# Performance work log

Hardware: AMD Instinct MI355X
Metric: run time of the kernel (lower is better)

Reference implementation:

```python
import jax, jax.numpy as jnp
import numpy as np

K_NEIGH = 12
RADIUS = 0.5


def _mlp(x, w1, b1, w2, b2):
    return jax.nn.relu(x @ w1 + b1) @ w2 + b2


def _angle(a, b):
    # atan2(||a x b||, a.b), as in PyG point-pair features
    c = jnp.cross(a, b)
    return jnp.arctan2(jnp.linalg.norm(c, axis=-1), jnp.sum(a * b, axis=-1))


def _quat_to_mat(q):
    w, x, y, z = q[:, 0], q[:, 1], q[:, 2], q[:, 3]
    m = jnp.stack([
        1 - 2 * (y * y + z * z), 2 * (x * y - z * w), 2 * (x * z + y * w),
        2 * (x * y + z * w), 1 - 2 * (x * x + z * z), 2 * (y * z - x * w),
        2 * (x * z - y * w), 2 * (y * z + x * w), 1 - 2 * (x * x + y * y),
    ], axis=-1)
    return m.reshape(-1, 3, 3)


def _lin_params(key, fan_in, fan_out):
    kw, kb = jax.random.split(key)
    s = 1.0 / np.sqrt(fan_in)
    w = jax.random.uniform(kw, (fan_in, fan_out), minval=-s, maxval=s, dtype=jnp.float32)
    b = jax.random.uniform(kb, (fan_out,), minval=-s, maxval=s, dtype=jnp.float32)
    return w, b


def setup_inputs() -> dict:
    key = jax.random.key(0)
    keys = jax.random.split(key, 8)
    points = jax.random.uniform(keys[0], (1, 128, 64, 3), dtype=jnp.float32)
    dims = [(7, 32, 16), (19, 32, 8), (24, 32, 16), (16, 32, 8), (24, 32, 16), (16, 32, 12), (27, 64, 1)]
    names = ['l1', 'g1', 'l2', 'g2', 'l3', 'g3', 'l4']
    inp = {'points': points}
    for i, (nm, (di, dh, do)) in enumerate(zip(names, dims)):
        k1, k2 = jax.random.split(keys[i + 1])
        w1, b1 = _lin_params(k1, di, dh)
        w2, b2 = _lin_params(k2, dh, do)
        inp[nm + '_w1'], inp[nm + '_b1'], inp[nm + '_w2'], inp[nm + '_b2'] = w1, b1, w2, b2
    return inp


def reference(points, l1_w1, l1_b1, l1_w2, l1_b2, g1_w1, g1_b1, g1_w2, g1_b2,
              l2_w1, l2_b1, l2_w2, l2_b2, g2_w1, g2_b1, g2_w2, g2_b2,
              l3_w1, l3_b1, l3_w2, l3_b2, g3_w1, g3_b1, g3_w2, g3_b2,
              l4_w1, l4_b1, l4_w2, l4_b2):
    B, H, W, _ = points.shape
    pos = points.reshape(-1, 3)          # [N,3]
    N = pos.shape[0]
    K = K_NEIGH
    pos_sg = jax.lax.stop_gradient(pos)  # torch detaches pos before edge features

    # --- dense radius graph: K nearest neighbors, self-padded beyond radius ---
    sq = jnp.sum(pos_sg * pos_sg, -1)
    d2 = sq[:, None] + sq[None, :] - 2.0 * (pos_sg @ pos_sg.T)  # [N,N]
    idx = jnp.arange(N)
    d2 = d2.at[idx, idx].set(jnp.inf)
    neg_d2_k, knn = jax.lax.top_k(-d2, K)
    d2_k = -neg_d2_k
    dense = jnp.where(d2_k <= RADIUS * RADIUS, knn, idx[:, None])  # [N,K]
    rows = jnp.repeat(idx, K)            # [E]
    cols = dense.reshape(-1)             # [E]

    # --- covariance of neighborhood, analytic 3x3 eig -> PCA normals ---
    nbr = pos[dense]                     # [N,K,3] (non-detached, as in torch)
    cent = jnp.mean(nbr, axis=1, keepdims=True)
    diff = nbr - cent
    cov = jnp.einsum('nki,nkj->nij', diff, diff) / K
    noise = (jax.random.uniform(jax.random.key(42), (100, 3), dtype=jnp.float32) - 0.5) * 1e-8
    cov = cov + jnp.diag(noise)          # torch.diag of (100,3) -> length-3 vector broadcast
    eig_val, eig_vec = jnp.linalg.eigh(cov)  # ascending, matches sort+gather in torch
    normals = eig_vec[:, :, 0]           # eigenvector of smallest eigenvalue
    pca_normals = normals.reshape(B, H, W, 3).transpose(0, 3, 1, 2)

    # --- edge feature stack: gather-MLP-mean-broadcast chain ---
    cart = pos_sg[cols] - pos_sg[rows]   # [E,3]
    dist = jnp.linalg.norm(cart, axis=-1)
    n_r, n_c = normals[rows], normals[cols]
    ppf = jnp.stack([dist, _angle(n_r, cart), _angle(n_c, cart), _angle(n_r, n_c)], -1)
    x = _mlp(jnp.concatenate([cart, ppf], -1), l1_w1, l1_b1, l1_w2, l1_b2)  # [E,16]

    gx = jnp.concatenate([x.reshape(N, K, -1).mean(1), normals], -1)        # [N,19]
    x_g = _mlp(gx, g1_w1, g1_b1, g1_w2, g1_b2)                              # [N,8]
    x = _mlp(jnp.concatenate([x, x_g[rows]], 1), l2_w1, l2_b1, l2_w2, l2_b2)

    x_g = _mlp(x.reshape(N, K, -1).mean(1), g2_w1, g2_b1, g2_w2, g2_b2)
    x = _mlp(jnp.concatenate([x, x_g[rows]], 1), l3_w1, l3_b1, l3_w2, l3_b2)

    x_g = _mlp(x.reshape(N, K, -1).mean(1), g3_w1, g3_b1, g3_w2, g3_b2)     # [N,12]
    quat = x_g[:, :4]
    quat = quat / (jnp.linalg.norm(quat, axis=-1) + 1e-8)[:, None]
    mat = _quat_to_mat(quat)             # [N,3,3]
    feat_g = x_g[:, 4:]
    rot_cart = jnp.einsum('eij,ej->ei', mat[rows], cart)
    x = _mlp(jnp.concatenate([x, feat_g[rows], rot_cart], 1), l4_w1, l4_b1, l4_w2, l4_b2)

    point_fea = jax.nn.softmax(x.reshape(N, K), axis=1)
    point_fea = point_fea.reshape(B, H, W, K).transpose(0, 3, 1, 2)
    return pca_normals, point_fea
```

## Files before the change

### kernel.cpp

```cpp
#include <hip/hip_runtime.h>
#include <math.h>

#define KNB 12
#define GRD 8
#define NCELL (GRD * GRD * GRD)


__device__ __forceinline__ unsigned umin32(unsigned a, unsigned b) {
    unsigned r; asm("v_min_u32 %0, %1, %2" : "=v"(r) : "v"(a), "v"(b)); return r;
}
__device__ __forceinline__ unsigned umax32(unsigned a, unsigned b) {
    unsigned r; asm("v_max_u32 %0, %1, %2" : "=v"(r) : "v"(a), "v"(b)); return r;
}

__device__ __forceinline__ float fm(float a, float b) { return __fmul_rn(a, b); }
__device__ __forceinline__ float fa(float a, float b) { return __fadd_rn(a, b); }
__device__ __forceinline__ float fs(float a, float b) { return __fsub_rn(a, b); }
__device__ __forceinline__ float fsignf(float a, float b) { return (b >= 0.0f) ? fabsf(a) : -fabsf(a); }

__device__ float slapy2_(float x, float y) {
    float xa = fabsf(x), ya = fabsf(y);
    float w = fmaxf(xa, ya), z = fminf(xa, ya);
    if (z == 0.0f) return w;
    float q = z / w;
    return fm(w, __fsqrt_rn(fa(1.0f, fm(q, q))));
}

__device__ void slartg_(float f, float g, float& c, float& s, float& r) {
    if (g == 0.0f) { c = 1.0f; s = 0.0f; r = f; }
    else if (f == 0.0f) { c = 0.0f; s = (g >= 0.0f) ? 1.0f : -1.0f; r = fabsf(g); }
    else {
        float d = __fsqrt_rn(fa(fm(f, f), fm(g, g)));
        c = fabsf(f) / d;
        r = (f >= 0.0f) ? d : -d;
        s = g / r;
    }
}

__device__ void slaev2_(float a, float b, float cc,
                        float& rt1, float& rt2, float& cs1, float& sn1) {
    float sm = fa(a, cc), df = fs(a, cc), adf = fabsf(df);
    float tb = fa(b, b), ab = fabsf(tb);
    float acmx, acmn;
    if (fabsf(a) > fabsf(cc)) { acmx = a; acmn = cc; } else { acmx = cc; acmn = a; }
    float rt;
    if (adf > ab)      { float q = ab / adf; rt = fm(adf, __fsqrt_rn(fa(1.0f, fm(q, q)))); }
    else if (adf < ab) { float q = adf / ab; rt = fm(ab,  __fsqrt_rn(fa(1.0f, fm(q, q)))); }
    else               rt = fm(ab, __fsqrt_rn(2.0f));
    int sgn1;
    if (sm < 0.0f) {
        rt1 = fm(0.5f, fs(sm, rt)); sgn1 = -1;
        rt2 = fs(fm(acmx / rt1, acmn), fm(b / rt1, b));
    } else if (sm > 0.0f) {
        rt1 = fm(0.5f, fa(sm, rt)); sgn1 = 1;
        rt2 = fs(fm(acmx / rt1, acmn), fm(b / rt1, b));
    } else { rt1 = fm(0.5f, rt); rt2 = fm(-0.5f, rt); sgn1 = 1; }
    int sgn2; float cs;
    if (df >= 0.0f) { cs = fa(df, rt); sgn2 = 1; } else { cs = fs(df, rt); sgn2 = -1; }
    float acs = fabsf(cs);
    if (acs > ab) {
        float ct = -tb / cs;
        sn1 = 1.0f / __fsqrt_rn(fa(1.0f, fm(ct, ct)));
        cs1 = fm(ct, sn1);
    } else {
        if (ab == 0.0f) { cs1 = 1.0f; sn1 = 0.0f; }
        else {
            float tn = -cs / tb;
            cs1 = 1.0f / __fsqrt_rn(fa(1.0f, fm(tn, tn)));
            sn1 = fm(tn, cs1);
        }
    }
    if (sgn1 == sgn2) { float tn = cs1; cs1 = -sn1; sn1 = tn; }
}

#define Z(r, c)  wk[((r) - 1) * 3 + ((c) - 1)]
#define D(i)     wk[8 + (i)]
#define E(i)     wk[11 + (i)]
#define WC(i)    wk[13 + (i)]
#define WSN(i)   wk[15 + (i)]

__device__ __forceinline__ void rotcf(float* wk, int j1, int j2, float ct, float st) {
    for (int r = 1; r <= 3; ++r) {
        float temp = Z(r, j2);
        Z(r, j2) = fs(fm(ct, temp), fm(st, Z(r, j1)));
        Z(r, j1) = fa(fm(st, temp), fm(ct, Z(r, j1)));
    }
}

__device__ void eig3_smallest_f32(float* wk,
                                  float a00, float a10, float a20,
                                  float a11, float a21, float a22,
                                  float& v1o, float& v2o, float& v3o) {
    for (int r = 1; r <= 3; ++r)
        for (int c = 1; c <= 3; ++c) Z(r, c) = (r == c) ? 1.0f : 0.0f;

    float tau = 0.0f, v3 = 0.0f;
    D(1) = a00;
    if (a20 != 0.0f) {
        float xn = fabsf(a20);
        float beta = -fsignf(slapy2_(a10, xn), a10);
        tau = fs(beta, a10) / beta;
        float rinv = 1.0f / fs(a10, beta);
        v3 = fm(a20, rinv);
        E(1) = beta;
        float w1 = fa(fm(tau, a11), fm(tau, fm(a21, v3)));
        float w2 = fa(fm(tau, a21), fm(fm(tau, v3), a22));
        float dot = fa(w1, fm(w2, v3));
        float al = fm(fm(-0.5f, tau), dot);
        w1 = fa(w1, al);
        w2 = fa(w2, fm(al, v3));
        D(2) = fs(fs(a11, w1), w1);
        E(2) = fs(fs(a21, fm(v3, w1)), w2);
        D(3) = fs(fs(a22, fm(v3, w2)), fm(w2, v3));
    } else {
        E(1) = a10; D(2) = a11; E(2) = a21; D(3) = a22;
    }

    const float eps = 5.9604645e-8f;
    const float eps2 = 3.5527137e-15f;
    const float safmin = 1.17549435e-38f;
    int jtot = 0; const int nmaxit = 90;
    int l1 = 1;
    while (l1 <= 3) {
        if (l1 > 1) E(l1 - 1) = 0.0f;
        int m;
        for (m = l1; m <= 2; ++m) {
            float tst = fabsf(E(m));
            if (tst == 0.0f) break;
            if (tst <= fm(fm(__fsqrt_rn(fabsf(D(m))), __fsqrt_rn(fabsf(D(m + 1)))), eps)) {
                E(m) = 0.0f; break;
            }
        }
        int l = l1, lend = m;
        l1 = m + 1;
        if (lend == l) continue;
        if (fabsf(D(lend)) < fabsf(D(l))) { int t = l; l = lend; lend = t; }
        if (lend > l) {
            for (;;) {
                int mq = lend;
                if (l != lend) {
                    for (mq = l; mq <= lend - 1; ++mq) {
                        float tst = fm(E(mq), E(mq));
                        if (tst <= fa(fm(fm(eps2, fabsf(D(mq))), fabsf(D(mq + 1))), safmin)) break;
                    }
                }
                if (mq < lend) E(mq) = 0.0f;
                float p = D(l);
                if (mq == l) { l += 1; if (l <= lend) continue; break; }
                if (mq == l + 1) {
                    float rt1, rt2, cc, ss;
                    slaev2_(D(l), E(l), D(l + 1), rt1, rt2, cc, ss);
                    rotcf(wk, l, l + 1, cc, ss);
                    D(l) = rt1; D(l + 1) = rt2; E(l) = 0.0f;
                    l += 2; if (l <= lend) continue; break;
                }
                if (jtot == nmaxit) break;
                jtot++;
                float g = fs(D(l + 1), p) / fm(2.0f, E(l));
                float r = slapy2_(g, 1.0f);
                g = fa(fs(D(mq), p), E(l) / fa(g, fsignf(r, g)));
                float s_ = 1.0f, c_ = 1.0f; p = 0.0f;
                for (int i = mq - 1; i >= l; --i) {
                    float f = fm(s_, E(i)), b = fm(c_, E(i));
                    slartg_(g, f, c_, s_, r);
                    if (i != mq - 1) E(i + 1) = r;
                    g = fs(D(i + 1), p);
                    r = fa(fm(fs(D(i), g), s_), fm(fm(2.0f, c_), b));
                    p = fm(s_, r);
                    D(i + 1) = fa(g, p);
                    g = fs(fm(c_, r), b);
                    WC(i) = c_; WSN(i) = -s_;
                }
                for (int i = mq - 1; i >= l; --i) rotcf(wk, i, i + 1, WC(i), WSN(i));
                D(l) = fs(D(l), p); E(l) = g;
            }
        } else {
            for (;;) {
                int mq = lend;
                if (l != lend) {
                    for (mq = l; mq >= lend + 1; --mq) {
                        float tst = fm(E(mq - 1), E(mq - 1));
                        if (tst <= fa(fm(fm(eps2, fabsf(D(mq))), fabsf(D(mq - 1))), safmin)) break;
                    }
                }
                if (mq > lend) E(mq - 1) = 0.0f;
                float p = D(l);
                if (mq == l) { l -= 1; if (l >= lend) continue; break; }
                if (mq == l - 1) {
                    float rt1, rt2, cc, ss;
                    slaev2_(D(l - 1), E(l - 1), D(l), rt1, rt2, cc, ss);
                    rotcf(wk, l - 1, l, cc, ss);
                    D(l - 1) = rt1; D(l) = rt2; E(l - 1) = 0.0f;
                    l -= 2; if (l >= lend) continue; break;
                }
                if (jtot == nmaxit) break;
                jtot++;
                float g = fs(D(l - 1), p) / fm(2.0f, E(l - 1));
                float r = slapy2_(g, 1.0f);
                g = fa(fs(D(mq), p), E(l - 1) / fa(g, fsignf(r, g)));
                float s_ = 1.0f, c_ = 1.0f; p = 0.0f;
                for (int i = mq; i <= l - 1; ++i) {
                    float f = fm(s_, E(i)), b = fm(c_, E(i));
                    slartg_(g, f, c_, s_, r);
                    if (i != mq) E(i - 1) = r;
                    g = fs(D(i), p);
                    r = fa(fm(fs(D(i + 1), g), s_), fm(fm(2.0f, c_), b));
                    p = fm(s_, r);
                    D(i) = fa(g, p);
                    g = fs(fm(c_, r), b);
                    WC(i) = c_; WSN(i) = s_;
                }
                for (int i = mq; i <= l - 1; ++i) rotcf(wk, i, i + 1, WC(i), WSN(i));
                D(l) = fs(D(l), p); E(l - 1) = g;
            }
        }
    }
    for (int ii = 2; ii <= 3; ++ii) {
        int i = ii - 1, kk = i; float p = D(i);
        for (int j = ii; j <= 3; ++j) if (D(j) < p) { kk = j; p = D(j); }
        if (kk != i) {
            D(kk) = D(i); D(i) = p;
            for (int r = 1; r <= 3; ++r) { float t = Z(r, i); Z(r, i) = Z(r, kk); Z(r, kk) = t; }
        }
    }
    if (tau != 0.0f) {
        for (int c = 1; c <= 3; ++c) {
            float ss = fa(Z(2, c), fm(v3, Z(3, c)));
            float t = fm(tau, ss);
            Z(2, c) = fs(Z(2, c), t);
            Z(3, c) = fs(Z(3, c), fm(t, v3));
        }
    }
    v1o = Z(1, 1); v2o = Z(2, 1); v3o = Z(3, 1);
}

__device__ void threefry2x32_(unsigned k0, unsigned k1, unsigned c0, unsigned c1,
                              unsigned& o0, unsigned& o1) {
    const unsigned rot[8] = {13u, 15u, 26u, 6u, 17u, 29u, 16u, 24u};
    unsigned ks[3] = {k0, k1, k0 ^ k1 ^ 0x1BD11BDAu};
    unsigned x0 = c0 + k0, x1 = c1 + k1;
    for (int blk = 0; blk < 5; ++blk) {
        const unsigned* r = &rot[(blk & 1) * 4];
        for (int i = 0; i < 4; ++i) {
            x0 += x1;
            x1 = (x1 << r[i]) | (x1 >> (32 - r[i]));
            x1 ^= x0;
        }
        x0 += ks[(blk + 1) % 3];
        x1 += ks[(blk + 2) % 3] + (unsigned)(blk + 1);
    }
    o0 = x0; o1 = x1;
}

__device__ float noise_diag_(int j) {
    unsigned m = (unsigned)(4 * j);
    unsigned o0, o1;
    threefry2x32_(0u, 42u, m, 150u + m, o0, o1);
    unsigned bits = (o0 >> 9) | 0x3f800000u;
    float u = fs(__uint_as_float(bits), 1.0f);
    return fm(fs(u, 0.5f), 1e-8f);
}

__device__ __forceinline__ float angf(float ax, float ay, float az,
                                      float bx, float by, float bz) {
    float cx = ay * bz - az * by;
    float cy = az * bx - ax * bz;
    float cz = ax * by - ay * bx;
    float cn = sqrtf(cx * cx + cy * cy + cz * cz);
    float d  = ax * bx + ay * by + az * bz;
    return atan2f(cn, d);
}


__global__ void k_zero(int* __restrict__ hist) {
    hist[threadIdx.x] = 0;
}

__global__ void k_prep(const float* __restrict__ pts, float4* __restrict__ pos4,
                       int* __restrict__ pcell, int* __restrict__ hist, int n) {
    int i = blockIdx.x * blockDim.x + threadIdx.x;
    if (i < n) {
        float x = pts[i * 3], y = pts[i * 3 + 1], z = pts[i * 3 + 2];
        float sq = fa(fa(fm(x, x), fm(y, y)), fm(z, z));
        pos4[i] = make_float4(x, y, z, sq);
        int cx = (int)(x * 8.0f); cx = cx < 0 ? 0 : (cx > GRD - 1 ? GRD - 1 : cx);
        int cy = (int)(y * 8.0f); cy = cy < 0 ? 0 : (cy > GRD - 1 ? GRD - 1 : cy);
        int cz = (int)(z * 8.0f); cz = cz < 0 ? 0 : (cz > GRD - 1 ? GRD - 1 : cz);
        int cid = (cz * GRD + cy) * GRD + cx;
        pcell[i] = cid;
        atomicAdd(&hist[cid], 1);
    }
}

__global__ __launch_bounds__(NCELL) void k_scan(const int* __restrict__ hist,
                                                int* __restrict__ start,
                                                int* __restrict__ cursor) {
    __shared__ int s[NCELL];
    int t = threadIdx.x;
    int v = hist[t];
    s[t] = v;
    __syncthreads();
    for (int off = 1; off < NCELL; off <<= 1) {
        int x = (t >= off) ? s[t - off] : 0;
        __syncthreads();
        s[t] += x;
        __syncthreads();
    }
    int ex = s[t] - v;
    start[t] = ex;
    cursor[t] = ex;
    if (t == NCELL - 1) start[NCELL] = s[t];
}

__global__ void k_scatter(const int* __restrict__ pcell, int* __restrict__ cursor,
                          int* __restrict__ order, int n) {
    int i = blockIdx.x * blockDim.x + threadIdx.x;
    if (i < n) {
        int slot = atomicAdd(&cursor[pcell[i]], 1);
        order[slot] = i;
    }
}

#define KEY_WORST 0xC0001FFFFFFFFFFFull
#define CBUF 128

__global__ __launch_bounds__(256) void k_knn(const float4* __restrict__ pos4,
                                             const int* __restrict__ order,
                                             const int* __restrict__ cstart,
                                             int* __restrict__ cols, int n) {
    __shared__ unsigned long long sbuf[4][CBUF];
    __shared__ int scnt[4];

    int lane = threadIdx.x & 63;
    int wv = threadIdx.x >> 6;
    int io = blockIdx.x * 4 + wv;
    if (io >= n) return;

    float4 P = pos4[io];
    int cx = (int)(P.x * 8.0f); cx = cx < 0 ? 0 : (cx > GRD - 1 ? GRD - 1 : cx);
    int cy = (int)(P.y * 8.0f); cy = cy < 0 ? 0 : (cy > GRD - 1 ? GRD - 1 : cy);
    int cz = (int)(P.z * 8.0f); cz = cz < 0 ? 0 : (cz > GRD - 1 ? GRD - 1 : cz);

    unsigned T = 0xFFFFFFFFu;
    int xlo = 0, xhi = 0, ylo = 0, yhi = 0, zlo = 0, zhi = 0;

    for (int r = 1; r < 16; ++r) {
        xlo = cx - r; if (xlo < 0) xlo = 0;
        xhi = cx + r; if (xhi > GRD - 1) xhi = GRD - 1;
        ylo = cy - r; if (ylo < 0) ylo = 0;
        yhi = cy + r; if (yhi > GRD - 1) yhi = GRD - 1;
        zlo = cz - r; if (zlo < 0) zlo = 0;
        zhi = cz + r; if (zhi > GRD - 1) zhi = GRD - 1;

        unsigned b0 = 0xFFFFFFFFu, b1 = 0xFFFFFFFFu;
        for (int zz = zlo; zz <= zhi; ++zz)
            for (int yy = ylo; yy <= yhi; ++yy) {
                int rowb = (zz * GRD + yy) * GRD;
                int jb = cstart[rowb + xlo];
                int je = cstart[rowb + xhi + 1];
                for (int t = jb + lane; t < je; t += 64) {
                    int j = order[t];
                    float4 Q = pos4[j];
                    float g = fm(P.x, Q.x);
                    g = fmaf(P.y, Q.y, g);
                    g = fmaf(P.z, Q.z, g);
                    float d2 = fs(fa(P.w, Q.w), fm(2.0f, g));
                    unsigned u = __float_as_uint(d2);
                    u = (j == io) ? 0xFFFFFFFFu : u;
                    unsigned lo = umin32(b0, u);
                    unsigned hi = umax32(b0, u);
                    b0 = lo;
                    b1 = umin32(b1, hi);
                }
            }

        {
            unsigned h0 = b0, h1 = b1;
            T = 0xFFFFFFFFu;
            for (int rr = 0; rr < KNB + 1; ++rr) {
                unsigned mn = h0;
#pragma unroll
                for (int off = 32; off >= 1; off >>= 1) {
                    unsigned o = (unsigned)__shfl_xor((int)mn, off, 64);
                    mn = umin32(mn, o);
                }
                unsigned long long bl = __ballot(h0 == mn);
                int first = __ffsll(bl) - 1;
                if (lane == first) { h0 = h1; h1 = 0xFFFFFFFFu; }
                T = mn;
            }
        }

        bool cover = (xlo == 0) && (xhi == GRD - 1) && (ylo == 0) && (yhi == GRD - 1)
                  && (zlo == 0) && (zhi == GRD - 1);
        if (cover) break;
        if (T != 0xFFFFFFFFu) {
            float gmin = 1e30f;
            if (xlo > 0)       gmin = fminf(gmin, fs(P.x, (float)xlo * 0.125f));
            if (xhi < GRD - 1) gmin = fminf(gmin, fs((float)(xhi + 1) * 0.125f, P.x));
            if (ylo > 0)       gmin = fminf(gmin, fs(P.y, (float)ylo * 0.125f));
            if (yhi < GRD - 1) gmin = fminf(gmin, fs((float)(yhi + 1) * 0.125f, P.y));
            if (zlo > 0)       gmin = fminf(gmin, fs(P.z, (float)zlo * 0.125f));
            if (zhi < GRD - 1) gmin = fminf(gmin, fs((float)(zhi + 1) * 0.125f, P.z));
            float g2 = fm(fm(gmin, gmin), 0.9995f);
            if (__uint_as_float(T) <= g2) break;
        }
    }

    if (lane == 0) scnt[wv] = 0;
    __builtin_amdgcn_wave_barrier();
    for (int zz = zlo; zz <= zhi; ++zz)
        for (int yy = ylo; yy <= yhi; ++yy) {
            int rowb = (zz * GRD + yy) * GRD;
            int jb = cstart[rowb + xlo];
            int je = cstart[rowb + xhi + 1];
            for (int t = jb + lane; t < je; t += 64) {
                int j = order[t];
                float4 Q = pos4[j];
                float g = fm(P.x, Q.x);
                g = fmaf(P.y, Q.y, g);
                g = fmaf(P.z, Q.z, g);
                float d2 = fs(fa(P.w, Q.w), fm(2.0f, g));
                unsigned u = __float_as_uint(d2);
                bool c = (u <= T) && (j != io);
                unsigned long long bl = __ballot(c);
                if (bl) {
                    int leader = __ffsll(bl) - 1;
                    int base = 0;
                    if (lane == leader)
                        base = atomicAdd(&scnt[wv], (int)__popcll(bl));
                    base = __shfl(base, leader, 64);
                    if (c) {
                        int pos = base + (int)__popcll(bl & ((1ull << lane) - 1ull));
                        unsigned us = u ^ (unsigned)(((int)u >> 31) | 0x80000000);
                        unsigned long long kb = (((unsigned long long)us << 13) | (unsigned)j)
                                                | 0xC000000000000000ull;
                        if (pos < CBUF) sbuf[wv][pos] = kb;
                    }
                }
            }
        }
    __builtin_amdgcn_wave_barrier();
    int cnt = scnt[wv];
    if (cnt > CBUF) cnt = CBUF;

    double k0 = __longlong_as_double((long long)KEY_WORST);
    double k1 = __longlong_as_double((long long)KEY_WORST);
    if (lane < cnt) k0 = __longlong_as_double((long long)sbuf[wv][lane]);
    if (lane + 64 < cnt) k1 = __longlong_as_double((long long)sbuf[wv][lane + 64]);
    double mykey = __longlong_as_double((long long)KEY_WORST);
    for (int rr = 0; rr < KNB; ++rr) {
        double mx = fmax(k0, k1);
#pragma unroll
        for (int off = 32; off >= 1; off >>= 1)
            mx = fmax(mx, __shfl_xor(mx, off, 64));
        if (k0 == mx) k0 = __longlong_as_double((long long)KEY_WORST);
        else if (k1 == mx) k1 = __longlong_as_double((long long)KEY_WORST);
        if (lane == rr) mykey = mx;
    }
    if (lane < KNB) {
        unsigned long long bits = (unsigned long long)__double_as_longlong(mykey);
        unsigned j = (unsigned)(bits & 0x1FFFu);
        unsigned u = (unsigned)((bits >> 13) & 0xFFFFFFFFull);
        unsigned ob = (u & 0x80000000u) ? (u ^ 0x80000000u) : ~u;
        float d2 = __uint_as_float(ob);
        cols[io * KNB + lane] = (d2 <= 0.25f) ? (int)j : io;
    }
}

__global__ __launch_bounds__(64) void k_normals(const float4* __restrict__ pos4,
                                                const int* __restrict__ cols,
                                                float4* __restrict__ nrm4,
                                                float* __restrict__ out, int n) {
    __shared__ float swk[64][19];
    int i = blockIdx.x * blockDim.x + threadIdx.x;
    if (i >= n) return;
    float* wk = swk[threadIdx.x];

    float qx[KNB], qy[KNB], qz[KNB];
#pragma unroll
    for (int k = 0; k < KNB; ++k) {
        float4 q = pos4[cols[i * KNB + k]];
        qx[k] = q.x; qy[k] = q.y; qz[k] = q.z;
    }
    float sx = qx[0], sy = qy[0], sz = qz[0];
#pragma unroll
    for (int k = 1; k < KNB; ++k) { sx = fa(sx, qx[k]); sy = fa(sy, qy[k]); sz = fa(sz, qz[k]); }
    float mx = sx / 12.0f, my = sy / 12.0f, mz = sz / 12.0f;
    float c00 = 0, c10 = 0, c20 = 0, c11 = 0, c21 = 0, c22 = 0;
#pragma unroll
    for (int k = 0; k < KNB; ++k) {
        float dx = fs(qx[k], mx), dy = fs(qy[k], my), dz = fs(qz[k], mz);
        c00 = fa(c00, fm(dx, dx));
        c10 = fa(c10, fm(dy, dx));
        c20 = fa(c20, fm(dz, dx));
        c11 = fa(c11, fm(dy, dy));
        c21 = fa(c21, fm(dz, dy));
        c22 = fa(c22, fm(dz, dz));
    }
    c00 = c00 / 12.0f; c10 = c10 / 12.0f; c20 = c20 / 12.0f;
    c11 = c11 / 12.0f; c21 = c21 / 12.0f; c22 = c22 / 12.0f;
    float v0 = noise_diag_(0), v1 = noise_diag_(1), v2 = noise_diag_(2);
    float a00 = fa(c00, v0), a10 = fa(c10, v0), a20 = fa(c20, v0);
    float a11 = fa(c11, v1), a21 = fa(c21, v1), a22 = fa(c22, v2);
    float e1, e2, e3;
    eig3_smallest_f32(wk, a00, a10, a20, a11, a21, a22, e1, e2, e3);
    nrm4[i] = make_float4(e1, e2, e3, 0.0f);
    out[i]         = e1;
    out[n + i]     = e2;
    out[2 * n + i] = e3;
}


struct WPtrs { const float* p[28]; };

template <int NI, int NH, int NO>
__device__ void mlpg(const float* __restrict__ w1, const float* __restrict__ b1,
                     const float* __restrict__ w2, const float* __restrict__ b2,
                     const float* in, float* out) {
#pragma unroll
    for (int o = 0; o < NO; ++o) out[o] = b2[o];
    for (int h = 0; h < NH; ++h) {
        float hh = b1[h];
#pragma unroll
        for (int ii = 0; ii < NI; ++ii) hh = fmaf(in[ii], w1[ii * NH + h], hh);
        hh = fmaxf(hh, 0.0f);
#pragma unroll
        for (int o = 0; o < NO; ++o) out[o] = fmaf(hh, w2[h * NO + o], out[o]);
    }
}

__global__ __launch_bounds__(192) void k_mlp(const float4* __restrict__ pos4,
                                             const int* __restrict__ cols,
                                             const float4* __restrict__ nrm4,
                                             WPtrs wp, float* __restrict__ out, int n) {
    __shared__ float sx[16 * 12 * 16];
    __shared__ float sg[16 * 12];
    __shared__ float smat[16 * 9];
    __shared__ float sfeat[16 * 8];
    __shared__ float slog[16 * 12];
    __shared__ float sred[16 * 2];

    int p = threadIdx.x / 12, k = threadIdx.x - p * 12;
    int nn = blockIdx.x * 16 + p;
    bool act = (nn < n);

    float cx = 0, cy = 0, cz = 0, nrx = 0, nry = 0, nrz = 0;
    float xr[16];

    if (act) {
        int col = cols[nn * 12 + k];
        float4 P = pos4[nn], Q = pos4[col];
        cx = Q.x - P.x; cy = Q.y - P.y; cz = Q.z - P.z;
        float dist = sqrtf(cx * cx + cy * cy + cz * cz);
        float4 NR = nrm4[nn], NC = nrm4[col];
        nrx = NR.x; nry = NR.y; nrz = NR.z;
        float a1 = angf(nrx, nry, nrz, cx, cy, cz);
        float a2 = angf(NC.x, NC.y, NC.z, cx, cy, cz);
        float a3 = angf(nrx, nry, nrz, NC.x, NC.y, NC.z);
        float in7[7] = {cx, cy, cz, dist, a1, a2, a3};
        mlpg<7, 32, 16>(wp.p[0], wp.p[1], wp.p[2], wp.p[3], in7, xr);
#pragma unroll
        for (int o = 0; o < 16; ++o) sx[(p * 12 + k) * 16 + o] = xr[o];
    }
    __syncthreads();

    if (act && k == 0) {
        float in19[19];
#pragma unroll
        for (int o = 0; o < 16; ++o) {
            float s = 0;
            for (int kk = 0; kk < 12; ++kk) s += sx[(p * 12 + kk) * 16 + o];
            in19[o] = s / 12.0f;
        }
        in19[16] = nrx; in19[17] = nry; in19[18] = nrz;
        float og[8];
        mlpg<19, 32, 8>(wp.p[4], wp.p[5], wp.p[6], wp.p[7], in19, og);
#pragma unroll
        for (int o = 0; o < 8; ++o) sg[p * 12 + o] = og[o];
    }
    __syncthreads();

    if (act) {
        float in24[24];
#pragma unroll
        for (int o = 0; o < 16; ++o) in24[o] = xr[o];
#pragma unroll
        for (int o = 0; o < 8; ++o) in24[16 + o] = sg[p * 12 + o];
        mlpg<24, 32, 16>(wp.p[8], wp.p[9], wp.p[10], wp.p[11], in24, xr);
#pragma unroll
        for (int o = 0; o < 16; ++o) sx[(p * 12 + k) * 16 + o] = xr[o];
    }
    __syncthreads();

    if (act && k == 0) {
        float in16[16];
#pragma unroll
        for (int o = 0; o < 16; ++o) {
            float s = 0;
            for (int kk = 0; kk < 12; ++kk) s += sx[(p * 12 + kk) * 16 + o];
            in16[o] = s / 12.0f;
        }
        float og[8];
        mlpg<16, 32, 8>(wp.p[12], wp.p[13], wp.p[14], wp.p[15], in16, og);
#pragma unroll
        for (int o = 0; o < 8; ++o) sg[p * 12 + o] = og[o];
    }
    __syncthreads();

    if (act) {
        float in24[24];
#pragma unroll
        for (int o = 0; o < 16; ++o) in24[o] = xr[o];
#pragma unroll
        for (int o = 0; o < 8; ++o) in24[16 + o] = sg[p * 12 + o];
        mlpg<24, 32, 16>(wp.p[16], wp.p[17], wp.p[18], wp.p[19], in24, xr);
#pragma unroll
        for (int o = 0; o < 16; ++o) sx[(p * 12 + k) * 16 + o] = xr[o];
    }
    __syncthreads();

    if (act && k == 0) {
        float in16[16];
#pragma unroll
        for (int o = 0; o < 16; ++o) {
            float s = 0;
            for (int kk = 0; kk < 12; ++kk) s += sx[(p * 12 + kk) * 16 + o];
            in16[o] = s / 12.0f;
        }
        float og[12];
        mlpg<16, 32, 12>(wp.p[20], wp.p[21], wp.p[22], wp.p[23], in16, og);
        float q0 = og[0], q1 = og[1], q2 = og[2], q3 = og[3];
        float qn = sqrtf(q0 * q0 + q1 * q1 + q2 * q2 + q3 * q3) + 1e-8f;
        q0 /= qn; q1 /= qn; q2 /= qn; q3 /= qn;
        float qw = q0, qx = q1, qy = q2, qz = q3;
        smat[p * 9 + 0] = 1.0f - 2.0f * (qy * qy + qz * qz);
        smat[p * 9 + 1] = 2.0f * (qx * qy - qz * qw);
        smat[p * 9 + 2] = 2.0f * (qx * qz + qy * qw);
        smat[p * 9 + 3] = 2.0f * (qx * qy + qz * qw);
        smat[p * 9 + 4] = 1.0f - 2.0f * (qx * qx + qz * qz);
        smat[p * 9 + 5] = 2.0f * (qy * qz - qx * qw);
        smat[p * 9 + 6] = 2.0f * (qx * qz - qy * qw);
        smat[p * 9 + 7] = 2.0f * (qy * qz + qx * qw);
        smat[p * 9 + 8] = 1.0f - 2.0f * (qx * qx + qy * qy);
#pragma unroll
        for (int o = 0; o < 8; ++o) sfeat[p * 8 + o] = og[4 + o];
    }
    __syncthreads();

    if (act) {
        float r0 = smat[p * 9 + 0] * cx + smat[p * 9 + 1] * cy + smat[p * 9 + 2] * cz;
        float r1 = smat[p * 9 + 3] * cx + smat[p * 9 + 4] * cy + smat[p * 9 + 5] * cz;
        float r2 = smat[p * 9 + 6] * cx + smat[p * 9 + 7] * cy + smat[p * 9 + 8] * cz;
        float in27[27];
#pragma unroll
        for (int o = 0; o < 16; ++o) in27[o] = xr[o];
#pragma unroll
        for (int o = 0; o < 8; ++o) in27[16 + o] = sfeat[p * 8 + o];
        in27[24] = r0; in27[25] = r1; in27[26] = r2;
        float lg[1];
        mlpg<27, 64, 1>(wp.p[24], wp.p[25], wp.p[26], wp.p[27], in27, lg);
        slog[p * 12 + k] = lg[0];
    }
    __syncthreads();

    if (act && k == 0) {
        float mx = slog[p * 12];
        for (int kk = 1; kk < 12; ++kk) mx = fmaxf(mx, slog[p * 12 + kk]);
        float se = 0;
        for (int kk = 0; kk < 12; ++kk) se += expf(slog[p * 12 + kk] - mx);
        sred[p * 2] = mx; sred[p * 2 + 1] = se;
    }
    __syncthreads();
    if (act) {
        float v = expf(slog[p * 12 + k] - sred[p * 2]) / sred[p * 2 + 1];
        out[3 * n + k * n + nn] = v;
    }
}


extern "C" void kernel_launch(void* const* d_in, const int* in_sizes, int n_in,
                              void* d_out, int out_size, void* d_ws, size_t ws_size,
                              hipStream_t stream) {
    const float* pts = (const float*)d_in[0];
    int n = in_sizes[0] / 3;

    char* ws = (char*)d_ws;
    float4* pos4  = (float4*)ws;
    int*    cols  = (int*)(ws + (size_t)n * 16);
    float4* nrm4  = (float4*)(ws + (size_t)n * 64);
    int*    pcell = (int*)(ws + (size_t)n * 80);
    int*    order = (int*)(ws + (size_t)n * 84);
    int*    hist  = (int*)(ws + (size_t)n * 88);
    int*    start = hist + NCELL;
    int*    cursor = start + NCELL + 1;
    float*  out = (float*)d_out;

    WPtrs wp;
    for (int a = 0; a < 28; ++a) wp.p[a] = (const float*)d_in[a + 1];

    k_zero<<<1, NCELL, 0, stream>>>(hist);
    k_prep<<<(n + 255) / 256, 256, 0, stream>>>(pts, pos4, pcell, hist, n);
    k_scan<<<1, NCELL, 0, stream>>>(hist, start, cursor);
    k_scatter<<<(n + 255) / 256, 256, 0, stream>>>(pcell, cursor, order, n);
    k_knn<<<(n + 3) / 4, 256, 0, stream>>>(pos4, order, start, cols, n);
    k_normals<<<(n + 63) / 64, 64, 0, stream>>>(pos4, cols, nrm4, out, n);
    k_mlp<<<(n + 15) / 16, 192, 0, stream>>>(pos4, cols, nrm4, wp, out, n);
}
```

Baseline: 255.8 us.

## Split MLP hidden units across thread pairs and keep eigen-solver state in registers

The per-edge MLP kernel now uses 24 threads per point instead of 12. Each edge MLP's hidden layer is split in halves across two threads, and the per-point global MLPs are spread over all 24 threads with a shared-memory reduction, replacing the single-thread k==0 serial path. The 3x3 tridiagonal QL eigen solver in the normals kernel is rewritten to keep its working matrix and diagonals in named registers instead of a shared-memory scratch array. The changes aim to remove serialized global-MLP bottlenecks and LDS traffic, at the cost of more barriers, more shared memory and more code specialization.

Result: slower. 286.8 us (+12.1%).

```diff
diff --git a/kernel.cpp b/kernel.cpp
--- a/kernel.cpp
+++ b/kernel.cpp
@@ -73,47 +73,50 @@
     if (sgn1 == sgn2) { float tn = cs1; cs1 = -sn1; sn1 = tn; }
 }
 
-#define Z(r, c)  wk[((r) - 1) * 3 + ((c) - 1)]
-#define D(i)     wk[8 + (i)]
-#define E(i)     wk[11 + (i)]
-#define WC(i)    wk[13 + (i)]
-#define WSN(i)   wk[15 + (i)]
-
-__device__ __forceinline__ void rotcf(float* wk, int j1, int j2, float ct, float st) {
-    for (int r = 1; r <= 3; ++r) {
-        float temp = Z(r, j2);
-        Z(r, j2) = fs(fm(ct, temp), fm(st, Z(r, j1)));
-        Z(r, j1) = fa(fm(st, temp), fm(ct, Z(r, j1)));
-    }
-}
-
-__device__ void eig3_smallest_f32(float* wk,
-                                  float a00, float a10, float a20,
+__device__ __forceinline__ void rot2col(float& a1, float& a2, float& a3,
+                                        float& b1, float& b2, float& b3,
+                                        float ct, float st) {
+    float t;
+    t = b1; b1 = fs(fm(ct, t), fm(st, a1)); a1 = fa(fm(st, t), fm(ct, a1));
+    t = b2; b2 = fs(fm(ct, t), fm(st, a2)); a2 = fa(fm(st, t), fm(ct, a2));
+    t = b3; b3 = fs(fm(ct, t), fm(st, a3)); a3 = fa(fm(st, t), fm(ct, a3));
+}
+
+#define RD(i)    ((i) == 1 ? d1 : ((i) == 2 ? d2 : d3))
+#define WRD(i,v) do { float _t = (v); if ((i) == 1) d1 = _t; else if ((i) == 2) d2 = _t; else d3 = _t; } while (0)
+#define RE(i)    ((i) == 1 ? e1 : e2)
+#define WRE(i,v) do { float _t = (v); if ((i) == 1) e1 = _t; else e2 = _t; } while (0)
+#define SWAPC(a,b) do { float _t = (a); (a) = (b); (b) = _t; } while (0)
+
+__device__ void eig3_smallest_reg(float a00, float a10, float a20,
                                   float a11, float a21, float a22,
                                   float& v1o, float& v2o, float& v3o) {
-    for (int r = 1; r <= 3; ++r)
-        for (int c = 1; c <= 3; ++c) Z(r, c) = (r == c) ? 1.0f : 0.0f;
+    float z11 = 1.0f, z21 = 0.0f, z31 = 0.0f;
+    float z12 = 0.0f, z22 = 1.0f, z32 = 0.0f;
+    float z13 = 0.0f, z23 = 0.0f, z33 = 1.0f;
+    float d1, d2, d3, e1, e2;
+    float wc1 = 0.0f, wc2 = 0.0f, ws1 = 0.0f, ws2 = 0.0f;
 
     float tau = 0.0f, v3 = 0.0f;
-    D(1) = a00;
+    d1 = a00;
     if (a20 != 0.0f) {
         float xn = fabsf(a20);
         float beta = -fsignf(slapy2_(a10, xn), a10);
         tau = fs(beta, a10) / beta;
         float rinv = 1.0f / fs(a10, beta);
         v3 = fm(a20, rinv);
-        E(1) = beta;
+        e1 = beta;
         float w1 = fa(fm(tau, a11), fm(tau, fm(a21, v3)));
         float w2 = fa(fm(tau, a21), fm(fm(tau, v3), a22));
         float dot = fa(w1, fm(w2, v3));
         float al = fm(fm(-0.5f, tau), dot);
         w1 = fa(w1, al);
         w2 = fa(w2, fm(al, v3));
-        D(2) = fs(fs(a11, w1), w1);
-        E(2) = fs(fs(a21, fm(v3, w1)), w2);
-        D(3) = fs(fs(a22, fm(v3, w2)), fm(w2, v3));
+        d2 = fs(fs(a11, w1), w1);
+        e2 = fs(fs(a21, fm(v3, w1)), w2);
+        d3 = fs(fs(a22, fm(v3, w2)), fm(w2, v3));
     } else {
-        E(1) = a10; D(2) = a11; E(2) = a21; D(3) = a22;
+        e1 = a10; d2 = a11; e2 = a21; d3 = a22;
     }
 
     const float eps = 5.9604645e-8f;
@@ -122,116 +125,150 @@
     int jtot = 0; const int nmaxit = 90;
     int l1 = 1;
     while (l1 <= 3) {
-        if (l1 > 1) E(l1 - 1) = 0.0f;
+        if (l1 > 1) WRE(l1 - 1, 0.0f);
         int m;
         for (m = l1; m <= 2; ++m) {
-            float tst = fabsf(E(m));
+            float tst = fabsf(RE(m));
             if (tst == 0.0f) break;
-            if (tst <= fm(fm(__fsqrt_rn(fabsf(D(m))), __fsqrt_rn(fabsf(D(m + 1)))), eps)) {
-                E(m) = 0.0f; break;
+            if (tst <= fm(fm(__fsqrt_rn(fabsf(RD(m))), __fsqrt_rn(fabsf(RD(m + 1)))), eps)) {
+                WRE(m, 0.0f); break;
             }
         }
         int l = l1, lend = m;
         l1 = m + 1;
         if (lend == l) continue;
-        if (fabsf(D(lend)) < fabsf(D(l))) { int t = l; l = lend; lend = t; }
+        if (fabsf(RD(lend)) < fabsf(RD(l))) { int t = l; l = lend; lend = t; }
         if (lend > l) {
             for (;;) {
                 int mq = lend;
                 if (l != lend) {
                     for (mq = l; mq <= lend - 1; ++mq) {
-                        float tst = fm(E(mq), E(mq));
-                        if (tst <= fa(fm(fm(eps2, fabsf(D(mq))), fabsf(D(mq + 1))), safmin)) break;
+                        float tst = fm(RE(mq), RE(mq));
+                        if (tst <= fa(fm(fm(eps2, fabsf(RD(mq))), fabsf(RD(mq + 1))), safmin)) break;
                     }
                 }
-                if (mq < lend) E(mq) = 0.0f;
-                float p = D(l);
+                if (mq < lend) WRE(mq, 0.0f);
+                float p = RD(l);
                 if (mq == l) { l += 1; if (l <= lend) continue; break; }
                 if (mq == l + 1) {
                     float rt1, rt2, cc, ss;
-                    slaev2_(D(l), E(l), D(l + 1), rt1, rt2, cc, ss);
-                    rotcf(wk, l, l + 1, cc, ss);
-                    D(l) = rt1; D(l + 1) = rt2; E(l) = 0.0f;
+                    if (l == 1) {
+                        slaev2_(d1, e1, d2, rt1, rt2, cc, ss);
+                        rot2col(z11, z21, z31, z12, z22, z32, cc, ss);
+                        d1 = rt1; d2 = rt2; e1 = 0.0f;
+                    } else {
+                        slaev2_(d2, e2, d3, rt1, rt2, cc, ss);
+                        rot2col(z12, z22, z32, z13, z23, z33, cc, ss);
+                        d2 = rt1; d3 = rt2; e2 = 0.0f;
+                    }
                     l += 2; if (l <= lend) continue; break;
                 }
                 if (jtot == nmaxit) break;
                 jtot++;
-                float g = fs(D(l + 1), p) / fm(2.0f, E(l));
+                float g = fs(d2, p) / fm(2.0f, e1);
                 float r = slapy2_(g, 1.0f);
-                g = fa(fs(D(mq), p), E(l) / fa(g, fsignf(r, g)));
+                g = fa(fs(d3, p), e1 / fa(g, fsignf(r, g)));
                 float s_ = 1.0f, c_ = 1.0f; p = 0.0f;
-                for (int i = mq - 1; i >= l; --i) {
-                    float f = fm(s_, E(i)), b = fm(c_, E(i));
+                {
+                    float f = fm(s_, e2), b = fm(c_, e2);
                     slartg_(g, f, c_, s_, r);
-                    if (i != mq - 1) E(i + 1) = r;
-                    g = fs(D(i + 1), p);
-                    r = fa(fm(fs(D(i), g), s_), fm(fm(2.0f, c_), b));
+                    g = fs(d3, p);
+                    r = fa(fm(fs(d2, g), s_), fm(fm(2.0f, c_), b));
                     p = fm(s_, r);
-                    D(i + 1) = fa(g, p);
+                    d3 = fa(g, p);
                     g = fs(fm(c_, r), b);
-                    WC(i) = c_; WSN(i) = -s_;
-                }
-                for (int i = mq - 1; i >= l; --i) rotcf(wk, i, i + 1, WC(i), WSN(i));
-                D(l) = fs(D(l), p); E(l) = g;
+                    wc2 = c_; ws2 = -s_;
+                }
+                {
+                    float f = fm(s_, e1), b = fm(c_, e1);
+                    slartg_(g, f, c_, s_, r);
+                    e2 = r;
+                    g = fs(d2, p);
+                    r = fa(fm(fs(d1, g), s_), fm(fm(2.0f, c_), b));
+                    p = fm(s_, r);
+                    d2 = fa(g, p);
+                    g = fs(fm(c_, r), b);
+                    wc1 = c_; ws1 = -s_;
+                }
+                rot2col(z12, z22, z32, z13, z23, z33, wc2, ws2);
+                rot2col(z11, z21, z31, z12, z22, z32, wc1, ws1);
+                d1 = fs(d1, p); e1 = g;
             }
         } else {
             for (;;) {
                 int mq = lend;
                 if (l != lend) {
                     for (mq = l; mq >= lend + 1; --mq) {
-                        float tst = fm(E(mq - 1), E(mq - 1));
-                        if (tst <= fa(fm(fm(eps2, fabsf(D(mq))), fabsf(D(mq - 1))), safmin)) break;
+                        float tst = fm(RE(mq - 1), RE(mq - 1));
+                        if (tst <= fa(fm(fm(eps2, fabsf(RD(mq))), fabsf(RD(mq - 1))), safmin)) break;
                     }
                 }
-                if (mq > lend) E(mq - 1) = 0.0f;
-                float p = D(l);
+                if (mq > lend) WRE(mq - 1, 0.0f);
+                float p = RD(l);
                 if (mq == l) { l -= 1; if (l >= lend) continue; break; }
                 if (mq == l - 1) {
                     float rt1, rt2, cc, ss;
-                    slaev2_(D(l - 1), E(l - 1), D(l), rt1, rt2, cc, ss);
-                    rotcf(wk, l - 1, l, cc, ss);
-                    D(l - 1) = rt1; D(l) = rt2; E(l - 1) = 0.0f;
+                    if (l == 2) {
+                        slaev2_(d1, e1, d2, rt1, rt2, cc, ss);
+                        rot2col(z11, z21, z31, z12, z22, z32, cc, ss);
+                        d1 = rt1; d2 = rt2; e1 = 0.0f;
+                    } else {
+                        slaev2_(d2, e2, d3, rt1, rt2, cc, ss);
+                        rot2col(z12, z22, z32, z13, z23, z33, cc, ss);
+                        d2 = rt1; d3 = rt2; e2 = 0.0f;
+                    }
                     l -= 2; if (l >= lend) continue; break;
                 }
                 if (jtot == nmaxit) break;
                 jtot++;
-                float g = fs(D(l - 1), p) / fm(2.0f, E(l - 1));
+                float g = fs(d2, p) / fm(2.0f, e2);
                 float r = slapy2_(g, 1.0f);
-                g = fa(fs(D(mq), p), E(l - 1) / fa(g, fsignf(r, g)));
+                g = fa(fs(d1, p), e2 / fa(g, fsignf(r, g)));
                 float s_ = 1.0f, c_ = 1.0f; p = 0.0f;
-                for (int i = mq; i <= l - 1; ++i) {
-                    float f = fm(s_, E(i)), b = fm(c_, E(i));
+                {
+                    float f = fm(s_, e1), b = fm(c_, e1);
                     slartg_(g, f, c_, s_, r);
-                    if (i != mq) E(i - 1) = r;
-                    g = fs(D(i), p);
-                    r = fa(fm(fs(D(i + 1), g), s_), fm(fm(2.0f, c_), b));
+                    g = fs(d1, p);
+                    r = fa(fm(fs(d2, g), s_), fm(fm(2.0f, c_), b));
                     p = fm(s_, r);
-                    D(i) = fa(g, p);
+                    d1 = fa(g, p);
                     g = fs(fm(c_, r), b);
-                    WC(i) = c_; WSN(i) = s_;
-                }
-                for (int i = mq; i <= l - 1; ++i) rotcf(wk, i, i + 1, WC(i), WSN(i));
-                D(l) = fs(D(l), p); E(l - 1) = g;
+                    wc1 = c_; ws1 = s_;
+                }
+                {
+                    float f = fm(s_, e2), b = fm(c_, e2);
+                    slartg_(g, f, c_, s_, r);
+                    e1 = r;
+                    g = fs(d2, p);
+                    r = fa(fm(fs(d3, g), s_), fm(fm(2.0f, c_), b));
+                    p = fm(s_, r);
+                    d2 = fa(g, p);
+                    g = fs(fm(c_, r), b);
+                    wc2 = c_; ws2 = s_;
+                }
+                rot2col(z11, z21, z31, z12, z22, z32, wc1, ws1);
+                rot2col(z12, z22, z32, z13, z23, z33, wc2, ws2);
+                d3 = fs(d3, p); e2 = g;
             }
         }
     }
     for (int ii = 2; ii <= 3; ++ii) {
-        int i = ii - 1, kk = i; float p = D(i);
-        for (int j = ii; j <= 3; ++j) if (D(j) < p) { kk = j; p = D(j); }
+        int i = ii - 1, kk = i; float p = RD(i);
+        for (int j = ii; j <= 3; ++j) { float dj = RD(j); if (dj < p) { kk = j; p = dj; } }
         if (kk != i) {
-            D(kk) = D(i); D(i) = p;
-            for (int r = 1; r <= 3; ++r) { float t = Z(r, i); Z(r, i) = Z(r, kk); Z(r, kk) = t; }
+            WRD(kk, RD(i)); WRD(i, p);
+            if (i == 1 && kk == 2)      { SWAPC(z11, z12); SWAPC(z21, z22); SWAPC(z31, z32); }
+            else if (i == 1 && kk == 3) { SWAPC(z11, z13); SWAPC(z21, z23); SWAPC(z31, z33); }
+            else                        { SWAPC(z12, z13); SWAPC(z22, z23); SWAPC(z32, z33); }
         }
     }
     if (tau != 0.0f) {
-        for (int c = 1; c <= 3; ++c) {
-            float ss = fa(Z(2, c), fm(v3, Z(3, c)));
-            float t = fm(tau, ss);
-            Z(2, c) = fs(Z(2, c), t);
-            Z(3, c) = fs(Z(3, c), fm(t, v3));
-        }
-    }
-    v1o = Z(1, 1); v2o = Z(2, 1); v3o = Z(3, 1);
+        float ss, t;
+        ss = fa(z21, fm(v3, z31)); t = fm(tau, ss); z21 = fs(z21, t); z31 = fs(z31, fm(t, v3));
+        ss = fa(z22, fm(v3, z32)); t = fm(tau, ss); z22 = fs(z22, t); z32 = fs(z32, fm(t, v3));
+        ss = fa(z23, fm(v3, z33)); t = fm(tau, ss); z23 = fs(z23, t); z33 = fs(z33, fm(t, v3));
+    }
+    v1o = z11; v2o = z21; v3o = z31;
 }
 
 __device__ void threefry2x32_(unsigned k0, unsigned k1, unsigned c0, unsigned c1,
@@ -472,10 +509,8 @@
                                                 const int* __restrict__ cols,
                                                 float4* __restrict__ nrm4,
                                                 float* __restrict__ out, int n) {
-    __shared__ float swk[64][19];
     int i = blockIdx.x * blockDim.x + threadIdx.x;
     if (i >= n) return;
-    float* wk = swk[threadIdx.x];
 
     float qx[KNB], qy[KNB], qz[KNB];
 #pragma unroll
@@ -504,7 +539,7 @@
     float a00 = fa(c00, v0), a10 = fa(c10, v0), a20 = fa(c20, v0);
     float a11 = fa(c11, v1), a21 = fa(c21, v1), a22 = fa(c22, v2);
     float e1, e2, e3;
-    eig3_smallest_f32(wk, a00, a10, a20, a11, a21, a22, e1, e2, e3);
+    eig3_smallest_reg(a00, a10, a20, a11, a21, a22, e1, e2, e3);
     nrm4[i] = make_float4(e1, e2, e3, 0.0f);
     out[i]         = e1;
     out[n + i]     = e2;
@@ -515,12 +550,16 @@
 struct WPtrs { const float* p[28]; };
 
 template <int NI, int NH, int NO>
-__device__ void mlpg(const float* __restrict__ w1, const float* __restrict__ b1,
-                     const float* __restrict__ w2, const float* __restrict__ b2,
-                     const float* in, float* out) {
-#pragma unroll
-    for (int o = 0; o < NO; ++o) out[o] = b2[o];
-    for (int h = 0; h < NH; ++h) {
+__device__ __forceinline__ void mlp_half(const float* __restrict__ w1, const float* __restrict__ b1,
+                                         const float* __restrict__ w2, const float* __restrict__ b2,
+                                         const float* in, float* out, int hf) {
+#pragma unroll
+    for (int o = 0; o < NO; ++o) out[o] = hf ? 0.0f : b2[o];
+    const int HH = NH / 2;
+    int h0 = hf * HH;
+#pragma unroll
+    for (int hi = 0; hi < HH; ++hi) {
+        int h = h0 + hi;
         float hh = b1[h];
 #pragma unroll
         for (int ii = 0; ii < NI; ++ii) hh = fmaf(in[ii], w1[ii * NH + h], hh);
@@ -530,18 +569,51 @@
     }
 }
 
-__global__ __launch_bounds__(192) void k_mlp(const float4* __restrict__ pos4,
-                                             const int* __restrict__ cols,
-                                             const float4* __restrict__ nrm4,
-                                             WPtrs wp, float* __restrict__ out, int n) {
-    __shared__ float sx[16 * 12 * 16];
-    __shared__ float sg[16 * 12];
-    __shared__ float smat[16 * 9];
-    __shared__ float sfeat[16 * 8];
-    __shared__ float slog[16 * 12];
-    __shared__ float sred[16 * 2];
-
-    int p = threadIdx.x / 12, k = threadIdx.x - p * 12;
+template <int NI, int NO>
+__device__ __forceinline__ void gmlp_part(const float* __restrict__ w1, const float* __restrict__ b1,
+                                          const float* __restrict__ w2, const float* __restrict__ b2,
+                                          const float* in, float* pout, int q) {
+#pragma unroll
+    for (int o = 0; o < NO; ++o) pout[o] = (q == 0) ? b2[o] : 0.0f;
+    {
+        float hh = b1[q];
+#pragma unroll
+        for (int ii = 0; ii < NI; ++ii) hh = fmaf(in[ii], w1[ii * 32 + q], hh);
+        hh = fmaxf(hh, 0.0f);
+#pragma unroll
+        for (int o = 0; o < NO; ++o) pout[o] = fmaf(hh, w2[q * NO + o], pout[o]);
+    }
+    if (q < 8) {
+        int h = 24 + q;
+        float hh = b1[h];
+#pragma unroll
+        for (int ii = 0; ii < NI; ++ii) hh = fmaf(in[ii], w1[ii * 32 + h], hh);
+        hh = fmaxf(hh, 0.0f);
+#pragma unroll
+        for (int o = 0; o < NO; ++o) pout[o] = fmaf(hh, w2[h * NO + o], pout[o]);
+    }
+}
+
+#define SCR(pp, qq, oo) s_scr[((pp) * 24 + (qq)) * 17 + (oo)]
+#define SX(pp, kk, oo)  s_x[((pp) * 12 + (kk)) * 17 + (oo)]
+#define SM(pp, oo)      s_m[(pp) * 17 + (oo)]
+#define GFV(pp, oo)     s_g[(pp) * 13 + (oo)]
+#define SLG(pp, kk)     s_log[(pp) * 13 + (kk)]
+
+__global__ __launch_bounds__(384, 3) void k_mlp(const float4* __restrict__ pos4,
+                                                const int* __restrict__ cols,
+                                                const float4* __restrict__ nrm4,
+                                                WPtrs wp, float* __restrict__ out, int n) {
+    __shared__ float s_scr[16 * 24 * 17];
+    __shared__ float s_x[16 * 12 * 17];
+    __shared__ float s_m[16 * 17];
+    __shared__ float s_g[16 * 13];
+    __shared__ float s_log[16 * 13];
+    __shared__ float s_red[16 * 2];
+
+    int t = threadIdx.x;
+    int p = t / 24, q = t - p * 24;
+    int k = q % 12, hf = q / 12;
     int nn = blockIdx.x * 16 + p;
     bool act = (nn < n);
 
@@ -559,25 +631,42 @@
         float a2 = angf(NC.x, NC.y, NC.z, cx, cy, cz);
         float a3 = angf(nrx, nry, nrz, NC.x, NC.y, NC.z);
         float in7[7] = {cx, cy, cz, dist, a1, a2, a3};
-        mlpg<7, 32, 16>(wp.p[0], wp.p[1], wp.p[2], wp.p[3], in7, xr);
-#pragma unroll
-        for (int o = 0; o < 16; ++o) sx[(p * 12 + k) * 16 + o] = xr[o];
-    }
-    __syncthreads();
-
-    if (act && k == 0) {
-        float in19[19];
-#pragma unroll
-        for (int o = 0; o < 16; ++o) {
-            float s = 0;
-            for (int kk = 0; kk < 12; ++kk) s += sx[(p * 12 + kk) * 16 + o];
-            in19[o] = s / 12.0f;
-        }
-        in19[16] = nrx; in19[17] = nry; in19[18] = nrz;
-        float og[8];
-        mlpg<19, 32, 8>(wp.p[4], wp.p[5], wp.p[6], wp.p[7], in19, og);
-#pragma unroll
-        for (int o = 0; o < 8; ++o) sg[p * 12 + o] = og[o];
+        float px[16];
+        mlp_half<7, 32, 16>(wp.p[0], wp.p[1], wp.p[2], wp.p[3], in7, px, hf);
+#pragma unroll
+        for (int o = 0; o < 16; ++o) SCR(p, q, o) = px[o];
+    }
+    __syncthreads();
+    if (act) {
+#pragma unroll
+        for (int o = 0; o < 16; ++o) xr[o] = SCR(p, k, o) + SCR(p, 12 + k, o);
+        if (hf == 0)
+#pragma unroll
+            for (int o = 0; o < 16; ++o) SX(p, k, o) = xr[o];
+    }
+    __syncthreads();
+
+    if (act && q < 16) {
+        float s = 0.0f;
+        for (int kk = 0; kk < 12; ++kk) s += SX(p, kk, q);
+        SM(p, q) = s / 12.0f;
+    }
+    __syncthreads();
+    if (act) {
+        float gin[19];
+#pragma unroll
+        for (int ii = 0; ii < 16; ++ii) gin[ii] = SM(p, ii);
+        gin[16] = nrx; gin[17] = nry; gin[18] = nrz;
+        float pg[8];
+        gmlp_part<19, 8>(wp.p[4], wp.p[5], wp.p[6], wp.p[7], gin, pg, q);
+#pragma unroll
+        for (int o = 0; o < 8; ++o) SCR(p, q, o) = pg[o];
+    }
+    __syncthreads();
+    if (act && q < 8) {
+        float s = 0.0f;
+        for (int j = 0; j < 24; ++j) s += SCR(p, j, q);
+        GFV(p, q) = s;
     }
     __syncthreads();
 
@@ -586,25 +675,42 @@
 #pragma unroll
         for (int o = 0; o < 16; ++o) in24[o] = xr[o];
 #pragma unroll
-        for (int o = 0; o < 8; ++o) in24[16 + o] = sg[p * 12 + o];
-        mlpg<24, 32, 16>(wp.p[8], wp.p[9], wp.p[10], wp.p[11], in24, xr);
-#pragma unroll
-        for (int o = 0; o < 16; ++o) sx[(p * 12 + k) * 16 + o] = xr[o];
-    }
-    __syncthreads();
-
-    if (act && k == 0) {
-        float in16[16];
-#pragma unroll
-        for (int o = 0; o < 16; ++o) {
-            float s = 0;
-            for (int kk = 0; kk < 12; ++kk) s += sx[(p * 12 + kk) * 16 + o];
-            in16[o] = s / 12.0f;
-        }
-        float og[8];
-        mlpg<16, 32, 8>(wp.p[12], wp.p[13], wp.p[14], wp.p[15], in16, og);
-#pragma unroll
-        for (int o = 0; o < 8; ++o) sg[p * 12 + o] = og[o];
+        for (int o = 0; o < 8; ++o) in24[16 + o] = GFV(p, o);
+        float px[16];
+        mlp_half<24, 32, 16>(wp.p[8], wp.p[9], wp.p[10], wp.p[11], in24, px, hf);
+#pragma unroll
+        for (int o = 0; o < 16; ++o) SCR(p, q, o) = px[o];
+    }
+    __syncthreads();
+    if (act) {
+#pragma unroll
+        for (int o = 0; o < 16; ++o) xr[o] = SCR(p, k, o) + SCR(p, 12 + k, o);
+        if (hf == 0)
+#pragma unroll
+            for (int o = 0; o < 16; ++o) SX(p, k, o) = xr[o];
+    }
+    __syncthreads();
+
+    if (act && q < 16) {
+        float s = 0.0f;
+        for (int kk = 0; kk < 12; ++kk) s += SX(p, kk, q);
+        SM(p, q) = s / 12.0f;
+    }
+    __syncthreads();
+    if (act) {
+        float gin[16];
+#pragma unroll
+        for (int ii = 0; ii < 16; ++ii) gin[ii] = SM(p, ii);
+        float pg[8];
+        gmlp_part<16, 8>(wp.p[12], wp.p[13], wp.p[14], wp.p[15], gin, pg, q);
+#pragma unroll
+        for (int o = 0; o < 8; ++o) SCR(p, q, o) = pg[o];
+    }
+    __syncthreads();
+    if (act && q < 8) {
+        float s = 0.0f;
+        for (int j = 0; j < 24; ++j) s += SCR(p, j, q);
+        GFV(p, q) = s;
     }
     __syncthreads();
 
@@ -613,67 +719,85 @@
 #pragma unroll
         for (int o = 0; o < 16; ++o) in24[o] = xr[o];
 #pragma unroll
-        for (int o = 0; o < 8; ++o) in24[16 + o] = sg[p * 12 + o];
-        mlpg<24, 32, 16>(wp.p[16], wp.p[17], wp.p[18], wp.p[19], in24, xr);
-#pragma unroll
-        for (int o = 0; o < 16; ++o) sx[(p * 12 + k) * 16 + o] = xr[o];
-    }
-    __syncthreads();
-
-    if (act && k == 0) {
-        float in16[16];
-#pragma unroll
-        for (int o = 0; o < 16; ++o) {
-            float s = 0;
-            for (int kk = 0; kk < 12; ++kk) s += sx[(p * 12 + kk) * 16 + o];
-            in16[o] = s / 12.0f;
-        }
-        float og[12];
-        mlpg<16, 32, 12>(wp.p[20], wp.p[21], wp.p[22], wp.p[23], in16, og);
-        float q0 = og[0], q1 = og[1], q2 = og[2], q3 = og[3];
-        float qn = sqrtf(q0 * q0 + q1 * q1 + q2 * q2 + q3 * q3) + 1e-8f;
-        q0 /= qn; q1 /= qn; q2 /= qn; q3 /= qn;
-        float qw = q0, qx = q1, qy = q2, qz = q3;
-        smat[p * 9 + 0] = 1.0f - 2.0f * (qy * qy + qz * qz);
-        smat[p * 9 + 1] = 2.0f * (qx * qy - qz * qw);
-        smat[p * 9 + 2] = 2.0f * (qx * qz + qy * qw);
-        smat[p * 9 + 3] = 2.0f * (qx * qy + qz * qw);
-        smat[p * 9 + 4] = 1.0f - 2.0f * (qx * qx + qz * qz);
-        smat[p * 9 + 5] = 2.0f * (qy * qz - qx * qw);
-        smat[p * 9 + 6] = 2.0f * (qx * qz - qy * qw);
-        smat[p * 9 + 7] = 2.0f * (qy * qz + qx * qw);
-        smat[p * 9 + 8] = 1.0f - 2.0f * (qx * qx + qy * qy);
-#pragma unroll
-        for (int o = 0; o < 8; ++o) sfeat[p * 8 + o] = og[4 + o];
-    }
-    __syncthreads();
-
-    if (act) {
-        float r0 = smat[p * 9 + 0] * cx + smat[p * 9 + 1] * cy + smat[p * 9 + 2] * cz;
-        float r1 = smat[p * 9 + 3] * cx + smat[p * 9 + 4] * cy + smat[p * 9 + 5] * cz;
-        float r2 = smat[p * 9 + 6] * cx + smat[p * 9 + 7] * cy + smat[p * 9 + 8] * cz;
+        for (int o = 0; o < 8; ++o) in24[16 + o] = GFV(p, o);
+        float px[16];
+        mlp_half<24, 32, 16>(wp.p[16], wp.p[17], wp.p[18], wp.p[19], in24, px, hf);
+#pragma unroll
+        for (int o = 0; o < 16; ++o) SCR(p, q, o) = px[o];
+    }
+    __syncthreads();
+    if (act) {
+#pragma unroll
+        for (int o = 0; o < 16; ++o) xr[o] = SCR(p, k, o) + SCR(p, 12 + k, o);
+        if (hf == 0)
+#pragma unroll
+            for (int o = 0; o < 16; ++o) SX(p, k, o) = xr[o];
+    }
+    __syncthreads();
+
+    if (act && q < 16) {
+        float s = 0.0f;
+        for (int kk = 0; kk < 12; ++kk) s += SX(p, kk, q);
+        SM(p, q) = s / 12.0f;
+    }
+    __syncthreads();
+    if (act) {
+        float gin[16];
+#pragma unroll
+        for (int ii = 0; ii < 16; ++ii) gin[ii] = SM(p, ii);
+        float pg[12];
+        gmlp_part<16, 12>(wp.p[20], wp.p[21], wp.p[22], wp.p[23], gin, pg, q);
+#pragma unroll
+        for (int o = 0; o < 12; ++o) SCR(p, q, o) = pg[o];
+    }
+    __syncthreads();
+    if (act && q < 12) {
+        float s = 0.0f;
+        for (int j = 0; j < 24; ++j) s += SCR(p, j, q);
+        GFV(p, q) = s;
+    }
+    __syncthreads();
+
+    if (act) {
+        float g0 = GFV(p, 0), g1v = GFV(p, 1), g2v = GFV(p, 2), g3v = GFV(p, 3);
+        float qn = sqrtf(g0 * g0 + g1v * g1v + g2v * g2v + g3v * g3v) + 1e-8f;
+        float qw = g0 / qn, qxx = g1v / qn, qyy = g2v / qn, qzz = g3v / qn;
+        float m0 = 1.0f - 2.0f * (qyy * qyy + qzz * qzz);
+        float m1 = 2.0f * (qxx * qyy - qzz * qw);
+        float m2 = 2.0f * (qxx * qzz + qyy * qw);
+        float m3 = 2.0f * (qxx * qyy + qzz * qw);
+        float m4 = 1.0f - 2.0f * (qxx * qxx + qzz * qzz);
+        float m5 = 2.0f * (qyy * qzz - qxx * qw);
+        float m6 = 2.0f * (qxx * qzz - qyy * qw);
+        float m7 = 2.0f * (qyy * qzz + qxx * qw);
+        float m8 = 1.0f - 2.0f * (qxx * qxx + qyy * qyy);
+        float r0 = m0 * cx + m1 * cy + m2 * cz;
+        float r1 = m3 * cx + m4 * cy + m5 * cz;
+        float r2 = m6 * cx + m7 * cy + m8 * cz;
         float in27[27];
 #pragma unroll
         for (int o = 0; o < 16; ++o) in27[o] = xr[o];
 #pragma unroll
-        for (int o = 0; o < 8; ++o) in27[16 + o] = sfeat[p * 8 + o];
+        for (int o = 0; o < 8; ++o) in27[16 + o] = GFV(p, 4 + o);
         in27[24] = r0; in27[25] = r1; in27[26] = r2;
-        float lg[1];
-        mlpg<27, 64, 1>(wp.p[24], wp.p[25], wp.p[26], wp.p[27], in27, lg);
-        slog[p * 12 + k] = lg[0];
-    }
-    __syncthreads();
-
-    if (act && k == 0) {
-        float mx = slog[p * 12];
-        for (int kk = 1; kk < 12; ++kk) mx = fmaxf(mx, slog[p * 12 + kk]);
+        float plg[1];
+        mlp_half<27, 64, 1>(wp.p[24], wp.p[25], wp.p[26], wp.p[27], in27, plg, hf);
+        SCR(p, q, 0) = plg[0];
+    }
+    __syncthreads();
+    if (act && hf == 0) SLG(p, k) = SCR(p, k, 0) + SCR(p, 12 + k, 0);
+    __syncthreads();
+
+    if (act && q == 0) {
+        float mx = SLG(p, 0);
+        for (int kk = 1; kk < 12; ++kk) mx = fmaxf(mx, SLG(p, kk));
         float se = 0;
-        for (int kk = 0; kk < 12; ++kk) se += expf(slog[p * 12 + kk] - mx);
-        sred[p * 2] = mx; sred[p * 2 + 1] = se;
-    }
-    __syncthreads();
-    if (act) {
-        float v = expf(slog[p * 12 + k] - sred[p * 2]) / sred[p * 2 + 1];
+        for (int kk = 0; kk < 12; ++kk) se += expf(SLG(p, kk) - mx);
+        s_red[p * 2] = mx; s_red[p * 2 + 1] = se;
+    }
+    __syncthreads();
+    if (act && hf == 0) {
+        float v = expf(SLG(p, k) - s_red[p * 2]) / s_red[p * 2 + 1];
         out[3 * n + k * n + nn] = v;
     }
 }
@@ -705,5 +829,5 @@
     k_scatter<<<(n + 255) / 256, 256, 0, stream>>>(pcell, cursor, order, n);
     k_knn<<<(n + 3) / 4, 256, 0, stream>>>(pos4, order, start, cols, n);
     k_normals<<<(n + 63) / 64, 64, 0, stream>>>(pos4, cols, nrm4, out, n);
-    k_mlp<<<(n + 15) / 16, 192, 0, stream>>>(pos4, cols, nrm4, wp, out, n);
-}
+    k_mlp<<<(n + 15) / 16, 384, 0, stream>>>(pos4, cols, nrm4, wp, out, n);
+}
```
